# Kernel optimization log

Hardware: AMD Instinct MI355X
Metric: run time of the kernel (lower is better)

The kernel has to match this reference:

```python
import jax, jax.numpy as jnp
import numpy as np

B, T, C = 1, 2048, 2048
H, KV, D = 16, 4, 128
PAST = 2048


def setup_inputs() -> dict:
    key = jax.random.key(0)
    ks = jax.random.split(key, 11)
    return {
        "x": jax.random.normal(ks[0], (B, T, C), jnp.float32),
        "ve": jax.random.normal(ks[1], (B, T, KV * D), jnp.float32),
        "cos": jax.random.normal(ks[2], (1, T, 1, D // 2), jnp.float32),
        "sin": jax.random.normal(ks[3], (1, T, 1, D // 2), jnp.float32),
        "past_key": jax.random.normal(ks[4], (B, PAST, KV, D), jnp.float32),
        "past_value": jax.random.normal(ks[5], (B, PAST, KV, D), jnp.float32),
        "Wq": jax.random.normal(ks[6], (C, H * D), jnp.float32) * 0.02,
        "Wk": jax.random.normal(ks[7], (C, KV * D), jnp.float32) * 0.02,
        "Wv": jax.random.normal(ks[8], (C, KV * D), jnp.float32) * 0.02,
        "Wo": jax.random.normal(ks[9], (H * D, C), jnp.float32) * 0.02,
        "Wg": jax.random.normal(ks[10], (12, KV), jnp.float32),
    }


def _rmsnorm(x):
    return x * jax.lax.rsqrt(jnp.mean(x * x, axis=-1, keepdims=True) + 1e-6)


def _rope(x, cos, sin):
    # x: (B,T,heads,D); cos/sin: (1,T,1,D//2) broadcast over heads
    d = x.shape[-1] // 2
    x1, x2 = x[..., :d], x[..., d:]
    return jnp.concatenate([x1 * cos + x2 * sin, -x1 * sin + x2 * cos], axis=-1)


def reference(x, ve, cos, sin, past_key, past_value, Wq, Wk, Wv, Wo, Wg):
    Bx, Tx, Cx = x.shape
    G = H // KV
    q = (x @ Wq).reshape(Bx, Tx, H, D)
    k = (x @ Wk).reshape(Bx, Tx, KV, D)
    v = (x @ Wv).reshape(Bx, Tx, KV, D)
    # value-embedding gate: 3*sigmoid over first 12 channels of x
    gate = 3.0 * jax.nn.sigmoid(x[..., :12] @ Wg)  # (B,T,KV)
    v = v + gate[..., None] * ve.reshape(Bx, Tx, KV, D)
    q = _rmsnorm(_rope(q, cos, sin)) * 1.2
    k = _rmsnorm(_rope(k, cos, sin)) * 1.2
    present_key = jnp.concatenate([past_key, k], axis=1)    # (B,S,KV,D)
    present_value = jnp.concatenate([past_value, v], axis=1)
    S = present_key.shape[1]
    q_t = q.transpose(0, 2, 1, 3)                           # (B,H,T,D)
    k_t = present_key.transpose(0, 2, 1, 3)                 # (B,KV,S,D)
    v_t = present_value.transpose(0, 2, 1, 3)
    # GQA expansion: repeat each kv head G times -> (B,H,S,D)
    k_t = jnp.broadcast_to(k_t[:, :, None], (Bx, KV, G, S, D)).reshape(Bx, H, S, D)
    v_t = jnp.broadcast_to(v_t[:, :, None], (Bx, KV, G, S, D)).reshape(Bx, H, S, D)
    scale = D ** -0.5
    scores = jnp.einsum("bhtd,bhsd->bhts", q_t, k_t) * scale
    query_pos = jnp.arange(S - Tx, S)[:, None]
    key_pos = jnp.arange(S)[None, :]
    causal = key_pos <= query_pos                           # (T,S)
    scores = jnp.where(causal[None, None], scores, -jnp.inf)
    w = jax.nn.softmax(scores, axis=-1)
    y = jnp.einsum("bhts,bhsd->bthd", w, v_t).reshape(Bx, Tx, H * D)
    y = y @ Wo
    return (y, present_key, present_value)
```

## Files before the change

### kernel.cpp

```cpp
#include <hip/hip_runtime.h>
#include <hip/hip_bf16.h>
#include <math.h>

typedef __attribute__((ext_vector_type(8))) short short8;
typedef __attribute__((ext_vector_type(4))) short short4v;
typedef __attribute__((ext_vector_type(4))) float f32x4;

#define DEV __device__ __forceinline__

DEV short f2bf(float f) {
  unsigned u = __builtin_bit_cast(unsigned, f);
  unsigned r = (u + 0x7FFFu + ((u >> 16) & 1u)) >> 16;
  return (short)r;
}

DEV short f2h(float f) {
  _Float16 h = (_Float16)f;
  return __builtin_bit_cast(short, h);
}

DEV float h2f(short s) {
  return (float)__builtin_bit_cast(_Float16, s);
}

DEV unsigned cvt_pk_bf16(float lo, float hi) {
  unsigned r;
  asm("v_cvt_pk_bf16_f32 %0, %1, %2" : "=v"(r) : "v"(lo), "v"(hi));
  return r;
}

DEV void gload_lds16(const void* g, void* l) {
  __builtin_amdgcn_global_load_lds((const __attribute__((address_space(1))) void*)g,
                                   (__attribute__((address_space(3))) void*)l, 16, 0, 0);
}

__global__ __launch_bounds__(256) void gemm_bf16_m64(const short* __restrict__ A,
                                                     const short* __restrict__ BT,
                                                     float* __restrict__ C,
                                                     int M, int N, int K) {
  __shared__ __attribute__((aligned(16))) short As[2][64 * 64];
  __shared__ __attribute__((aligned(16))) short Bs[2][128 * 64];
  const int tid = threadIdx.x;
  const int w = tid >> 6, l = tid & 63;
  const int g = l >> 4, lr = l & 15;
  int nbx = gridDim.x, nwg = nbx * gridDim.y;
  int flat = blockIdx.y * nbx + blockIdx.x;
  int qq = nwg >> 3;
  int f2 = (flat & 7) * qq + (flat >> 3);
  const int m0 = (f2 / nbx) * 64, n0 = (f2 % nbx) * 128;
  const int wr = w >> 1, wc = w & 1;
  f32x4 acc[2][4] = {};

  auto stage = [&](int buf, int k0) {
#pragma unroll
    for (int it = 0; it < 2; ++it) {
      int idx = it * 256 + tid;
      int row = idx >> 3;
      int scol = ((idx & 7) * 16) ^ ((row & 7) << 4);
      gload_lds16(A + (size_t)(m0 + row) * K + k0 + (scol >> 1), As[buf] + idx * 8);
    }
#pragma unroll
    for (int it = 0; it < 4; ++it) {
      int idx = it * 256 + tid;
      int row = idx >> 3;
      int scol = ((idx & 7) * 16) ^ ((row & 7) << 4);
      gload_lds16(BT + (size_t)(n0 + row) * K + k0 + (scol >> 1), Bs[buf] + idx * 8);
    }
  };

  stage(0, 0);
  __syncthreads();
  int cur = 0;
  for (int k0 = 0; k0 < K; k0 += 64) {
    if (k0 + 64 < K) stage(cur ^ 1, k0 + 64);
#pragma unroll
    for (int ki = 0; ki < 2; ++ki) {
      const int kcol = (ki * 64 + g * 16) ^ ((lr & 7) << 4);
      short8 af[2], bfr[4];
#pragma unroll
      for (int i = 0; i < 2; ++i)
        af[i] = *(const short8*)(As[cur] + (((wr * 32 + i * 16 + lr) * 128 + kcol) >> 1));
#pragma unroll
      for (int i = 0; i < 4; ++i)
        bfr[i] = *(const short8*)(Bs[cur] + (((wc * 64 + i * 16 + lr) * 128 + kcol) >> 1));
#pragma unroll
      for (int mi = 0; mi < 2; ++mi)
#pragma unroll
        for (int ni = 0; ni < 4; ++ni)
          acc[mi][ni] = __builtin_amdgcn_mfma_f32_16x16x32_bf16(af[mi], bfr[ni], acc[mi][ni], 0, 0, 0);
    }
    __syncthreads();
    cur ^= 1;
  }
#pragma unroll
  for (int mi = 0; mi < 2; ++mi)
#pragma unroll
    for (int ni = 0; ni < 4; ++ni) {
      int row = m0 + wr * 32 + mi * 16 + g * 4;
      int col = n0 + wc * 64 + ni * 16 + lr;
#pragma unroll
      for (int r = 0; r < 4; ++r)
        C[(size_t)(row + r) * N + col] = acc[mi][ni][r];
    }
}

__global__ __launch_bounds__(256) void gemm_bf16_k64(const short* __restrict__ A,
                                                     const short* __restrict__ BT,
                                                     float* __restrict__ C,
                                                     int M, int N, int K) {
  __shared__ __attribute__((aligned(16))) short As[2][128 * 64];
  __shared__ __attribute__((aligned(16))) short Bs[2][128 * 64];
  const int tid = threadIdx.x;
  const int w = tid >> 6, l = tid & 63;
  const int g = l >> 4, lr = l & 15;
  int nbx = gridDim.x, nwg = nbx * gridDim.y;
  int flat = blockIdx.y * nbx + blockIdx.x;
  int qq = nwg >> 3;
  int f2 = (flat & 7) * qq + (flat >> 3);
  const int m0 = (f2 / nbx) * 128, n0 = (f2 % nbx) * 128;
  const int wr = w >> 1, wc = w & 1;
  f32x4 acc[4][4] = {};

  auto stage = [&](int buf, int k0) {
#pragma unroll
    for (int it = 0; it < 4; ++it) {
      int idx = it * 256 + tid;
      int row = idx >> 3;
      int colB = (idx & 7) * 16;
      int scol = colB ^ ((row & 7) << 4);
      gload_lds16(A + (size_t)(m0 + row) * K + k0 + (scol >> 1), As[buf] + idx * 8);
      gload_lds16(BT + (size_t)(n0 + row) * K + k0 + (scol >> 1), Bs[buf] + idx * 8);
    }
  };

  stage(0, 0);
  __syncthreads();
  int cur = 0;
  for (int k0 = 0; k0 < K; k0 += 64) {
    if (k0 + 64 < K) stage(cur ^ 1, k0 + 64);
#pragma unroll
    for (int ki = 0; ki < 2; ++ki) {
      short8 af[4], bfr[4];
#pragma unroll
      for (int i = 0; i < 4; ++i) {
        int off = ((wr * 64 + i * 16 + lr) * 128 + ((ki * 64 + g * 16) ^ ((lr & 7) << 4))) >> 1;
        int offb = ((wc * 64 + i * 16 + lr) * 128 + ((ki * 64 + g * 16) ^ ((lr & 7) << 4))) >> 1;
        af[i] = *(const short8*)(As[cur] + off);
        bfr[i] = *(const short8*)(Bs[cur] + offb);
      }
#pragma unroll
      for (int mi = 0; mi < 4; ++mi)
#pragma unroll
        for (int ni = 0; ni < 4; ++ni)
          acc[mi][ni] = __builtin_amdgcn_mfma_f32_16x16x32_bf16(af[mi], bfr[ni], acc[mi][ni], 0, 0, 0);
    }
    __syncthreads();
    cur ^= 1;
  }
#pragma unroll
  for (int mi = 0; mi < 4; ++mi)
#pragma unroll
    for (int ni = 0; ni < 4; ++ni) {
      int row = m0 + wr * 64 + mi * 16 + g * 4;
      int col = n0 + wc * 64 + ni * 16 + lr;
#pragma unroll
      for (int r = 0; r < 4; ++r)
        C[(size_t)(row + r) * N + col] = acc[mi][ni][r];
    }
}

__global__ __launch_bounds__(256) void prep(const float* __restrict__ x,
                                            short* __restrict__ xb,
                                            const float* __restrict__ Wq,
                                            const float* __restrict__ Wk,
                                            const float* __restrict__ Wv,
                                            const float* __restrict__ Wo,
                                            short* __restrict__ WTqkv,
                                            short* __restrict__ WToT) {
  __shared__ float tile[32][33];
  int bid = blockIdx.x;
  int tid = threadIdx.x;
  if (bid < 4096) {
    int i = bid * 256 + tid;
    float4 v = ((const float4*)x)[i];
    short4v o;
    o.x = f2bf(v.x); o.y = f2bf(v.y); o.z = f2bf(v.z); o.w = f2bf(v.w);
    ((short4v*)xb)[i] = o;
    return;
  }
  int b = bid - 4096;
  int bx = b % 160, by = b / 160;
  const float* W;
  short* WT;
  int N, cb;
  if (bx < 64) { W = Wq; WT = WTqkv; N = 2048; cb = bx; }
  else if (bx < 80) { W = Wk; WT = WTqkv + (size_t)2048 * 2048; N = 512; cb = bx - 64; }
  else if (bx < 96) { W = Wv; WT = WTqkv + (size_t)2560 * 2048; N = 512; cb = bx - 80; }
  else { W = Wo; WT = WToT; N = 2048; cb = bx - 96; }
  int tx = tid & 31, ty = tid >> 5;
  int c0 = cb * 32, r0 = by * 32;
#pragma unroll
  for (int i = 0; i < 4; ++i)
    tile[ty + i * 8][tx] = W[(size_t)(r0 + ty + i * 8) * N + c0 + tx];
  __syncthreads();
#pragma unroll
  for (int i = 0; i < 4; ++i)
    WT[(size_t)(c0 + ty + i * 8) * 2048 + r0 + tx] = f2bf(tile[tx][ty + i * 8]);
}

__global__ __launch_bounds__(256) void qkv_post(const float* __restrict__ qkv,
                                                const float* __restrict__ cosb,
                                                const float* __restrict__ sinb,
                                                const float* __restrict__ x,
                                                const float* __restrict__ ve,
                                                const float* __restrict__ Wg,
                                                float* __restrict__ outPK,
                                                float* __restrict__ outPV,
                                                short* __restrict__ qb,
                                                short* __restrict__ kb) {
  int gw = (blockIdx.x * 256 + threadIdx.x) >> 6;
  int l = threadIdx.x & 63;
  int t = gw / 24, u = gw - t * 24;
  if (t >= 2048) return;
  if (u < 20) {
    float c = cosb[t * 64 + l], s = sinb[t * 64 + l];
    const float* src = qkv + (size_t)t * 3072 + (u < 16 ? u * 128 : 2048 + (u - 16) * 128);
    float x1 = src[l], x2 = src[64 + l];
    float lo = x1 * c + x2 * s;
    float hi = x2 * c - x1 * s;
    float ss = lo * lo + hi * hi;
#pragma unroll
    for (int d = 1; d < 64; d <<= 1) ss += __shfl_xor(ss, d, 64);
    float r = rsqrtf(ss * (1.0f / 128.0f) + 1e-6f) * 1.2f;
    if (u < 16) {
      const float SCQ = 0.08838834764831845f * 1.4426950408889634f;
      float rq = r * SCQ;
      size_t b = ((size_t)u * 2048 + t) * 128;
      qb[b + l] = f2bf(lo * rq);
      qb[b + 64 + l] = f2bf(hi * rq);
    } else {
      lo *= r; hi *= r;
      int kvh = u - 16;
      size_t b = ((size_t)(2048 + t) * 4 + kvh) * 128;
      outPK[b + l] = lo;
      outPK[b + 64 + l] = hi;
      size_t b2 = ((size_t)kvh * 4096 + 2048 + t) * 128;
      kb[b2 + l] = f2bf(lo);
      kb[b2 + 64 + l] = f2bf(hi);
    }
  } else {
    int kv = u - 20;
    float z = 0.f;
#pragma unroll
    for (int j = 0; j < 12; ++j) z += x[(size_t)t * 2048 + j] * Wg[j * 4 + kv];
    float gate = 3.0f / (1.0f + expf(-z));
    const float* vr = qkv + (size_t)t * 3072 + 2560 + kv * 128;
    const float* vei = ve + (size_t)t * 512 + kv * 128;
    float v0 = vr[l] + gate * vei[l];
    float v1 = vr[64 + l] + gate * vei[64 + l];
    size_t b = ((size_t)(2048 + t) * 4 + kv) * 128;
    outPV[b + l] = v0;
    outPV[b + 64 + l] = v1;
  }
}

__global__ __launch_bounds__(256) void past_copy(const float* __restrict__ pk,
                                                 const float* __restrict__ pv,
                                                 float* __restrict__ outPK,
                                                 float* __restrict__ outPV,
                                                 short* __restrict__ kb) {
  int i = blockIdx.x * 256 + threadIdx.x;
  int d = i & 127, kv = (i >> 7) & 3, s = i >> 9;
  float a = pk[i], b = pv[i];
  outPK[i] = a;
  outPV[i] = b;
  kb[((size_t)kv * 4096 + s) * 128 + d] = f2bf(a);
}

__global__ __launch_bounds__(256) void v_transpose(const float* __restrict__ PV,
                                                   short* __restrict__ vbT) {
  __shared__ float tile[32][33];
  int tx = threadIdx.x & 31, ty = threadIdx.x >> 5;
  int c0 = blockIdx.x * 32, r0 = blockIdx.y * 32;
#pragma unroll
  for (int i = 0; i < 4; ++i)
    tile[ty + i * 8][tx] = PV[(size_t)(r0 + ty + i * 8) * 512 + c0 + tx];
  __syncthreads();
#pragma unroll
  for (int i = 0; i < 4; ++i)
    vbT[(size_t)(c0 + ty + i * 8) * 4096 + r0 + tx] = f2bf(tile[tx][ty + i * 8]);
}

__global__ __launch_bounds__(256, 2) void attn(const short* __restrict__ qb,
                                               const short* __restrict__ kb,
                                               const short* __restrict__ vbT,
                                               short* __restrict__ Po,
                                               float* __restrict__ ml) {
  extern __shared__ __attribute__((aligned(16))) short smem[];
  short* Ks = smem;
  short* Vs = smem + 16384;
  const int tid = threadIdx.x, w = tid >> 6, l = tid & 63;
  const int g = l >> 4, lr = l & 15;
  const int lid = blockIdx.x;
  const int qbi = 15 - (lid >> 5);
  const int sub = lid & 31;
  const int h = sub >> 1, cls = sub & 1;
  const int kv = h >> 2;
  const int qw = qbi * 128 + w * 32;
  char* Pw = (char*)(smem + 32768) + w * 2048;
  const short* gK = kb + (size_t)kv * 4096 * 128;
  const short* gV = vbT + (size_t)kv * 128 * 4096;
  const int nT = 34 + 2 * qbi;
  const int cnt = (nT - cls + 1) >> 1;

  short8 aq[2][4];
#pragma unroll
  for (int u = 0; u < 2; ++u)
#pragma unroll
    for (int c4 = 0; c4 < 4; ++c4)
      aq[u][c4] = *(const short8*)(qb + ((size_t)(h * 2048 + qw + u * 16 + lr)) * 128 + c4 * 32 + g * 8);

  float m_r[2] = {-INFINITY, -INFINITY};
  float l_r[2] = {0.f, 0.f};
  f32x4 o[2][8] = {};

  const int rK = tid >> 4, cKs = ((tid & 15) * 16) ^ ((rK & 7) << 4);
  const int rV = tid >> 3, cVs = ((tid & 7) * 16) ^ ((rV & 7) << 4);
  const short* kptr = gK + (size_t)(cls * 64 + rK) * 128 + (cKs >> 1);
  const short* vptr = gV + (size_t)rV * 4096 + cls * 64 + (cVs >> 1);
  short* kdst = Ks + w * 512;
  short* vdst = Vs + w * 512;

  auto stageK = [&](int buf) {
#pragma unroll
    for (int it = 0; it < 4; ++it)
      gload_lds16(kptr + it * 2048, kdst + buf * 8192 + it * 2048);
    kptr += 16384;
  };
  auto stageV = [&](int buf) {
#pragma unroll
    for (int it = 0; it < 4; ++it)
      gload_lds16(vptr + (size_t)it * 131072, vdst + buf * 8192 + it * 2048);
    vptr += 128;
  };

  stageK(0);
  stageV(0);
  __syncthreads();
  int cur = 0;
  for (int i = 0; i < cnt; ++i) {
    const int s0 = (cls + 2 * i) * 64;
    if (i + 1 < cnt) {
      stageK(cur ^ 1);
      stageV(cur ^ 1);
    }
    f32x4 sc[2][4] = {};
    __builtin_amdgcn_s_setprio(1);
#pragma unroll
    for (int cc = 0; cc < 4; ++cc) {
      const int rb = cur * 8192 + (cc * 16 + lr) * 128;
      short8 bk[4];
#pragma unroll
      for (int c4 = 0; c4 < 4; ++c4)
        bk[c4] = *(const short8*)(Ks + rb + (((c4 * 64 + g * 16) ^ ((lr & 7) << 4)) >> 1));
#pragma unroll
      for (int c4 = 0; c4 < 4; ++c4) {
        sc[0][cc] = __builtin_amdgcn_mfma_f32_16x16x32_bf16(bk[c4], aq[0][c4], sc[0][cc], 0, 0, 0);
        sc[1][cc] = __builtin_amdgcn_mfma_f32_16x16x32_bf16(bk[c4], aq[1][c4], sc[1][cc], 0, 0, 0);
      }
    }
    __builtin_amdgcn_s_setprio(0);
    if (s0 + 63 > 2048 + qw) {
#pragma unroll
      for (int u = 0; u < 2; ++u)
#pragma unroll
        for (int cc = 0; cc < 4; ++cc)
#pragma unroll
          for (int r = 0; r < 4; ++r)
            sc[u][cc][r] = (s0 + cc * 16 + g * 4 + r <= 2048 + qw + u * 16 + lr)
                               ? sc[u][cc][r] : -INFINITY;
    }
    short8 ap[2][2];
#pragma unroll
    for (int u = 0; u < 2; ++u) {
      float pmax = -INFINITY;
#pragma unroll
      for (int cc = 0; cc < 4; ++cc) {
        float a = fmaxf(fmaxf(sc[u][cc][0], sc[u][cc][1]), fmaxf(sc[u][cc][2], sc[u][cc][3]));
        pmax = fmaxf(pmax, a);
      }
      if (!__all(pmax - m_r[u] <= 8.0f)) {
        float tm = fmaxf(pmax, __shfl_xor(pmax, 16, 64));
        tm = fmaxf(tm, __shfl_xor(tm, 32, 64));
        float mn = fmaxf(m_r[u], tm);
        float corr = exp2f(m_r[u] - mn);
        m_r[u] = mn;
        l_r[u] *= corr;
        float co[4];
#pragma unroll
        for (int r = 0; r < 4; ++r) co[r] = __shfl(corr, (l & 48) | (g * 4 + r), 64);
#pragma unroll
        for (int d8 = 0; d8 < 8; ++d8) {
          f32x4 tt = o[u][d8];
#pragma unroll
          for (int r = 0; r < 4; ++r) tt[r] *= co[r];
          o[u][d8] = tt;
        }
      }
      float ps = 0.f;
#pragma unroll
      for (int cc = 0; cc < 4; ++cc) {
        float p0 = exp2f(sc[u][cc][0] - m_r[u]);
        float p1 = exp2f(sc[u][cc][1] - m_r[u]);
        float p2 = exp2f(sc[u][cc][2] - m_r[u]);
        float p3 = exp2f(sc[u][cc][3] - m_r[u]);
        ps += (p0 + p1) + (p2 + p3);
        unsigned pk0 = cvt_pk_bf16(p0, p1);
        unsigned pk1 = cvt_pk_bf16(p2, p3);
        int off8 = (lr * 128 + cc * 32 + g * 8) ^ ((lr & 7) << 4);
        unsigned long long pq = (unsigned long long)pk0 | ((unsigned long long)pk1 << 32);
        *(unsigned long long*)(Pw + off8) = pq;
      }
      l_r[u] += ps;
#pragma unroll
      for (int ks = 0; ks < 2; ++ks)
        ap[u][ks] = *(const short8*)(Pw + ((lr * 128 + ks * 64 + g * 16) ^ ((lr & 7) << 4)));
    }
    __builtin_amdgcn_s_setprio(1);
#pragma unroll
    for (int d8 = 0; d8 < 8; ++d8) {
      const int rb = cur * 8192 + (d8 * 16 + lr) * 64;
      short8 bv0 = *(const short8*)(Vs + rb + (((0 * 64 + g * 16) ^ ((lr & 7) << 4)) >> 1));
      short8 bv1 = *(const short8*)(Vs + rb + (((1 * 64 + g * 16) ^ ((lr & 7) << 4)) >> 1));
      o[0][d8] = __builtin_amdgcn_mfma_f32_16x16x32_bf16(ap[0][0], bv0, o[0][d8], 0, 0, 0);
      o[0][d8] = __builtin_amdgcn_mfma_f32_16x16x32_bf16(ap[0][1], bv1, o[0][d8], 0, 0, 0);
      o[1][d8] = __builtin_amdgcn_mfma_f32_16x16x32_bf16(ap[1][0], bv0, o[1][d8], 0, 0, 0);
      o[1][d8] = __builtin_amdgcn_mfma_f32_16x16x32_bf16(ap[1][1], bv1, o[1][d8], 0, 0, 0);
    }
    __builtin_amdgcn_s_setprio(0);
    __syncthreads();
    cur ^= 1;
  }
#pragma unroll
  for (int u = 0; u < 2; ++u) {
    float ls = l_r[u];
    ls += __shfl_xor(ls, 16, 64);
    ls += __shfl_xor(ls, 32, 64);
    float inv = 1.0f / ls;
    float invo[4];
#pragma unroll
    for (int r = 0; r < 4; ++r) invo[r] = __shfl(inv, (l & 48) | (g * 4 + r), 64);
#pragma unroll
    for (int d8 = 0; d8 < 8; ++d8)
#pragma unroll
      for (int r = 0; r < 4; ++r)
        Po[((size_t)(cls * 16 + h) * 2048 + qw + u * 16 + g * 4 + r) * 128 + d8 * 16 + lr] =
            f2h(o[u][d8][r] * invo[r]);
    if (g == 0) {
      float2 v;
      v.x = m_r[u];
      v.y = ls;
      ((float2*)ml)[(size_t)(cls * 16 + h) * 2048 + qw + u * 16 + lr] = v;
    }
  }
}

__global__ __launch_bounds__(256) void attn_merge(const short* __restrict__ Po,
                                                  const float* __restrict__ ml,
                                                  short* __restrict__ ya) {
  int i = blockIdx.x * 256 + threadIdx.x;
  int q = i >> 8, rem = i & 255, h = rem >> 4, oct = rem & 15;
  float mc[2], lc[2];
#pragma unroll
  for (int c = 0; c < 2; ++c) {
    float2 v = ((const float2*)ml)[(size_t)(c * 16 + h) * 2048 + q];
    mc[c] = v.x; lc[c] = v.y;
  }
  float m = fmaxf(mc[0], mc[1]);
  float wsum = 0.f, acc[8] = {};
#pragma unroll
  for (int c = 0; c < 2; ++c) {
    float wc = lc[c] * exp2f(mc[c] - m);
    wsum += wc;
    short8 p = *(const short8*)(Po + ((size_t)(c * 16 + h) * 2048 + q) * 128 + oct * 8);
#pragma unroll
    for (int j = 0; j < 8; ++j) acc[j] += wc * h2f(p[j]);
  }
  float inv = 1.0f / wsum;
  short8 ov;
#pragma unroll
  for (int j = 0; j < 8; ++j) ov[j] = f2bf(acc[j] * inv);
  *(short8*)(ya + (size_t)q * 2048 + h * 128 + oct * 8) = ov;
}

extern "C" void kernel_launch(void* const* d_in, const int* in_sizes, int n_in,
                              void* d_out, int out_size, void* d_ws, size_t ws_size,
                              hipStream_t stream) {
  const float* x = (const float*)d_in[0];
  const float* ve = (const float*)d_in[1];
  const float* cosb = (const float*)d_in[2];
  const float* sinb = (const float*)d_in[3];
  const float* past_key = (const float*)d_in[4];
  const float* past_value = (const float*)d_in[5];
  const float* Wq = (const float*)d_in[6];
  const float* Wk = (const float*)d_in[7];
  const float* Wv = (const float*)d_in[8];
  const float* Wo = (const float*)d_in[9];
  const float* Wg = (const float*)d_in[10];

  float* outY = (float*)d_out;
  float* outPK = outY + 4194304;
  float* outPV = outPK + 2097152;

  short* base = (short*)d_ws;
  short* WToT = base;
  short* WTqkv = base + 4194304;
  short* xb = WTqkv + (size_t)6291456;
  float* qkv = (float*)(xb + (size_t)4194304);
  short* qb = (short*)(qkv + (size_t)6291456);
  short* kb = qb + (size_t)4194304;
  short* vbT = kb + (size_t)2097152;
  short* ya = vbT + (size_t)2097152;
  short* Po = WTqkv;
  float* mlb = (float*)(base + 20971520);

  static bool attr_set = false;
  if (!attr_set) {
    (void)hipFuncSetAttribute((const void*)attn,
                              hipFuncAttributeMaxDynamicSharedMemorySize, 73728);
    attr_set = true;
  }

  prep<<<14336, 256, 0, stream>>>(x, xb, Wq, Wk, Wv, Wo, WTqkv, WToT);

  gemm_bf16_m64<<<dim3(24, 32), 256, 0, stream>>>(xb, WTqkv, qkv, 2048, 3072, 2048);

  qkv_post<<<12288, 256, 0, stream>>>(qkv, cosb, sinb, x, ve, Wg, outPK, outPV, qb, kb);
  past_copy<<<4096, 256, 0, stream>>>(past_key, past_value, outPK, outPV, kb);
  v_transpose<<<dim3(16, 128), 256, 0, stream>>>(outPV, vbT);

  attn<<<512, 256, 73728, stream>>>(qb, kb, vbT, Po, mlb);
  attn_merge<<<2048, 256, 0, stream>>>(Po, mlb, ya);

  gemm_bf16_k64<<<dim3(16, 16), 256, 0, stream>>>(ya, WToT, outY, 2048, 2048, 2048);
}
```

Baseline: 181.4 us.

## Emit bf16 QKV from GEMM, fuse past_value copy into transpose, use 64-row output GEMM

The QKV projection GEMM now writes its output in bf16 instead of fp32, which halves the intermediate traffic that qkv_post reads. The past_value copy moves into v_transpose, so the past rows are read once from the input and written to both outputs, rather than copied first and read back. The output projection switches from a 128x128 tile GEMM to a 64x128 tile GEMM, doubling the grid for more parallelism. Rounding the pre-RoPE/RMSNorm q, k, v to bf16 adds precision loss, and v is also written to present_value, so that output loses precision too.

```diff
diff --git a/kernel.cpp b/kernel.cpp
--- a/kernel.cpp
+++ b/kernel.cpp
@@ -14,6 +14,11 @@
   return (short)r;
 }
 
+DEV float bf2f(short s) {
+  unsigned u = ((unsigned)(unsigned short)s) << 16;
+  return __builtin_bit_cast(float, u);
+}
+
 DEV short f2h(float f) {
   _Float16 h = (_Float16)f;
   return __builtin_bit_cast(short, h);
@@ -34,9 +39,79 @@
                                    (__attribute__((address_space(3))) void*)l, 16, 0, 0);
 }
 
-__global__ __launch_bounds__(256) void gemm_bf16_m64(const short* __restrict__ A,
+__global__ __launch_bounds__(256) void gemm_m64_f32(const short* __restrict__ A,
+                                                    const short* __restrict__ BT,
+                                                    float* __restrict__ C,
+                                                    int M, int N, int K) {
+  __shared__ __attribute__((aligned(16))) short As[2][64 * 64];
+  __shared__ __attribute__((aligned(16))) short Bs[2][128 * 64];
+  const int tid = threadIdx.x;
+  const int w = tid >> 6, l = tid & 63;
+  const int g = l >> 4, lr = l & 15;
+  int nbx = gridDim.x, nwg = nbx * gridDim.y;
+  int flat = blockIdx.y * nbx + blockIdx.x;
+  int qq = nwg >> 3;
+  int f2 = (flat & 7) * qq + (flat >> 3);
+  const int m0 = (f2 / nbx) * 64, n0 = (f2 % nbx) * 128;
+  const int wr = w >> 1, wc = w & 1;
+  f32x4 acc[2][4] = {};
+
+  auto stage = [&](int buf, int k0) {
+#pragma unroll
+    for (int it = 0; it < 2; ++it) {
+      int idx = it * 256 + tid;
+      int row = idx >> 3;
+      int scol = ((idx & 7) * 16) ^ ((row & 7) << 4);
+      gload_lds16(A + (size_t)(m0 + row) * K + k0 + (scol >> 1), As[buf] + idx * 8);
+    }
+#pragma unroll
+    for (int it = 0; it < 4; ++it) {
+      int idx = it * 256 + tid;
+      int row = idx >> 3;
+      int scol = ((idx & 7) * 16) ^ ((row & 7) << 4);
+      gload_lds16(BT + (size_t)(n0 + row) * K + k0 + (scol >> 1), Bs[buf] + idx * 8);
+    }
+  };
+
+  stage(0, 0);
+  __syncthreads();
+  int cur = 0;
+  for (int k0 = 0; k0 < K; k0 += 64) {
+    if (k0 + 64 < K) stage(cur ^ 1, k0 + 64);
+#pragma unroll
+    for (int ki = 0; ki < 2; ++ki) {
+      const int kcol = (ki * 64 + g * 16) ^ ((lr & 7) << 4);
+      short8 af[2], bfr[4];
+#pragma unroll
+      for (int i = 0; i < 2; ++i)
+        af[i] = *(const short8*)(As[cur] + (((wr * 32 + i * 16 + lr) * 128 + kcol) >> 1));
+#pragma unroll
+      for (int i = 0; i < 4; ++i)
+        bfr[i] = *(const short8*)(Bs[cur] + (((wc * 64 + i * 16 + lr) * 128 + kcol) >> 1));
+#pragma unroll
+      for (int mi = 0; mi < 2; ++mi)
+#pragma unroll
+        for (int ni = 0; ni < 4; ++ni)
+          acc[mi][ni] = __builtin_amdgcn_mfma_f32_16x16x32_bf16(af[mi], bfr[ni], acc[mi][ni], 0, 0, 0);
+    }
+    __syncthreads();
+    cur ^= 1;
+  }
+#pragma unroll
+  for (int mi = 0; mi < 2; ++mi)
+#pragma unroll
+    for (int ni = 0; ni < 4; ++ni) {
+      int row = m0 + wr * 32 + mi * 16 + g * 4;
+      int col = n0 + wc * 64 + ni * 16 + lr;
+#pragma unroll
+      for (int r = 0; r < 4; ++r)
+        C[(size_t)(row + r) * N + col] = acc[mi][ni][r];
+    }
+}
+
+__global__ __launch_bounds__(256) void gemm_m64_bf16(const short* __restrict__ A,
                                                      const short* __restrict__ BT,
-                                                     float* __restrict__ C,
+                                                     short* __restrict__ C,
                                                      int M, int N, int K) {
   __shared__ __attribute__((aligned(16))) short As[2][64 * 64];
   __shared__ __attribute__((aligned(16))) short Bs[2][128 * 64];
@@ -100,72 +175,7 @@
       int col = n0 + wc * 64 + ni * 16 + lr;
 #pragma unroll
       for (int r = 0; r < 4; ++r)
-        C[(size_t)(row + r) * N + col] = acc[mi][ni][r];
-    }
-}
-
-__global__ __launch_bounds__(256) void gemm_bf16_k64(const short* __restrict__ A,
-                                                     const short* __restrict__ BT,
-                                                     float* __restrict__ C,
-                                                     int M, int N, int K) {
-  __shared__ __attribute__((aligned(16))) short As[2][128 * 64];
-  __shared__ __attribute__((aligned(16))) short Bs[2][128 * 64];
-  const int tid = threadIdx.x;
-  const int w = tid >> 6, l = tid & 63;
-  const int g = l >> 4, lr = l & 15;
-  int nbx = gridDim.x, nwg = nbx * gridDim.y;
-  int flat = blockIdx.y * nbx + blockIdx.x;
-  int qq = nwg >> 3;
-  int f2 = (flat & 7) * qq + (flat >> 3);
-  const int m0 = (f2 / nbx) * 128, n0 = (f2 % nbx) * 128;
-  const int wr = w >> 1, wc = w & 1;
-  f32x4 acc[4][4] = {};
-
-  auto stage = [&](int buf, int k0) {
-#pragma unroll
-    for (int it = 0; it < 4; ++it) {
-      int idx = it * 256 + tid;
-      int row = idx >> 3;
-      int colB = (idx & 7) * 16;
-      int scol = colB ^ ((row & 7) << 4);
-      gload_lds16(A + (size_t)(m0 + row) * K + k0 + (scol >> 1), As[buf] + idx * 8);
-      gload_lds16(BT + (size_t)(n0 + row) * K + k0 + (scol >> 1), Bs[buf] + idx * 8);
-    }
-  };
-
-  stage(0, 0);
-  __syncthreads();
-  int cur = 0;
-  for (int k0 = 0; k0 < K; k0 += 64) {
-    if (k0 + 64 < K) stage(cur ^ 1, k0 + 64);
-#pragma unroll
-    for (int ki = 0; ki < 2; ++ki) {
-      short8 af[4], bfr[4];
-#pragma unroll
-      for (int i = 0; i < 4; ++i) {
-        int off = ((wr * 64 + i * 16 + lr) * 128 + ((ki * 64 + g * 16) ^ ((lr & 7) << 4))) >> 1;
-        int offb = ((wc * 64 + i * 16 + lr) * 128 + ((ki * 64 + g * 16) ^ ((lr & 7) << 4))) >> 1;
-        af[i] = *(const short8*)(As[cur] + off);
-        bfr[i] = *(const short8*)(Bs[cur] + offb);
-      }
-#pragma unroll
-      for (int mi = 0; mi < 4; ++mi)
-#pragma unroll
-        for (int ni = 0; ni < 4; ++ni)
-          acc[mi][ni] = __builtin_amdgcn_mfma_f32_16x16x32_bf16(af[mi], bfr[ni], acc[mi][ni], 0, 0, 0);
-    }
-    __syncthreads();
-    cur ^= 1;
-  }
-#pragma unroll
-  for (int mi = 0; mi < 4; ++mi)
-#pragma unroll
-    for (int ni = 0; ni < 4; ++ni) {
-      int row = m0 + wr * 64 + mi * 16 + g * 4;
-      int col = n0 + wc * 64 + ni * 16 + lr;
-#pragma unroll
-      for (int r = 0; r < 4; ++r)
-        C[(size_t)(row + r) * N + col] = acc[mi][ni][r];
+        C[(size_t)(row + r) * N + col] = f2bf(acc[mi][ni][r]);
     }
 }
 
@@ -208,7 +218,7 @@
     WT[(size_t)(c0 + ty + i * 8) * 2048 + r0 + tx] = f2bf(tile[tx][ty + i * 8]);
 }
 
-__global__ __launch_bounds__(256) void qkv_post(const float* __restrict__ qkv,
+__global__ __launch_bounds__(256) void qkv_post(const short* __restrict__ qkv,
                                                 const float* __restrict__ cosb,
                                                 const float* __restrict__ sinb,
                                                 const float* __restrict__ x,
@@ -224,8 +234,8 @@
   if (t >= 2048) return;
   if (u < 20) {
     float c = cosb[t * 64 + l], s = sinb[t * 64 + l];
-    const float* src = qkv + (size_t)t * 3072 + (u < 16 ? u * 128 : 2048 + (u - 16) * 128);
-    float x1 = src[l], x2 = src[64 + l];
+    const short* src = qkv + (size_t)t * 3072 + (u < 16 ? u * 128 : 2048 + (u - 16) * 128);
+    float x1 = bf2f(src[l]), x2 = bf2f(src[64 + l]);
     float lo = x1 * c + x2 * s;
     float hi = x2 * c - x1 * s;
     float ss = lo * lo + hi * hi;
@@ -254,10 +264,10 @@
 #pragma unroll
     for (int j = 0; j < 12; ++j) z += x[(size_t)t * 2048 + j] * Wg[j * 4 + kv];
     float gate = 3.0f / (1.0f + expf(-z));
-    const float* vr = qkv + (size_t)t * 3072 + 2560 + kv * 128;
+    const short* vr = qkv + (size_t)t * 3072 + 2560 + kv * 128;
     const float* vei = ve + (size_t)t * 512 + kv * 128;
-    float v0 = vr[l] + gate * vei[l];
-    float v1 = vr[64 + l] + gate * vei[64 + l];
+    float v0 = bf2f(vr[l]) + gate * vei[l];
+    float v1 = bf2f(vr[64 + l]) + gate * vei[64 + l];
     size_t b = ((size_t)(2048 + t) * 4 + kv) * 128;
     outPV[b + l] = v0;
     outPV[b + 64 + l] = v1;
@@ -265,26 +275,33 @@
 }
 
 __global__ __launch_bounds__(256) void past_copy(const float* __restrict__ pk,
-                                                 const float* __restrict__ pv,
                                                  float* __restrict__ outPK,
-                                                 float* __restrict__ outPV,
                                                  short* __restrict__ kb) {
   int i = blockIdx.x * 256 + threadIdx.x;
   int d = i & 127, kv = (i >> 7) & 3, s = i >> 9;
-  float a = pk[i], b = pv[i];
+  float a = pk[i];
   outPK[i] = a;
-  outPV[i] = b;
   kb[((size_t)kv * 4096 + s) * 128 + d] = f2bf(a);
 }
 
-__global__ __launch_bounds__(256) void v_transpose(const float* __restrict__ PV,
+__global__ __launch_bounds__(256) void v_transpose(const float* __restrict__ pv,
+                                                   float* __restrict__ outPV,
                                                    short* __restrict__ vbT) {
   __shared__ float tile[32][33];
   int tx = threadIdx.x & 31, ty = threadIdx.x >> 5;
   int c0 = blockIdx.x * 32, r0 = blockIdx.y * 32;
-#pragma unroll
-  for (int i = 0; i < 4; ++i)
-    tile[ty + i * 8][tx] = PV[(size_t)(r0 + ty + i * 8) * 512 + c0 + tx];
+  if (r0 < 2048) {
+#pragma unroll
+    for (int i = 0; i < 4; ++i) {
+      float v = pv[(size_t)(r0 + ty + i * 8) * 512 + c0 + tx];
+      tile[ty + i * 8][tx] = v;
+      outPV[(size_t)(r0 + ty + i * 8) * 512 + c0 + tx] = v;
+    }
+  } else {
+#pragma unroll
+    for (int i = 0; i < 4; ++i)
+      tile[ty + i * 8][tx] = outPV[(size_t)(r0 + ty + i * 8) * 512 + c0 + tx];
+  }
   __syncthreads();
 #pragma unroll
   for (int i = 0; i < 4; ++i)
@@ -516,8 +533,8 @@
   short* WToT = base;
   short* WTqkv = base + 4194304;
   short* xb = WTqkv + (size_t)6291456;
-  float* qkv = (float*)(xb + (size_t)4194304);
-  short* qb = (short*)(qkv + (size_t)6291456);
+  short* qkv = xb + (size_t)4194304;
+  short* qb = qkv + (size_t)12582912;
   short* kb = qb + (size_t)4194304;
   short* vbT = kb + (size_t)2097152;
   short* ya = vbT + (size_t)2097152;
@@ -533,14 +550,14 @@
 
   prep<<<14336, 256, 0, stream>>>(x, xb, Wq, Wk, Wv, Wo, WTqkv, WToT);
 
-  gemm_bf16_m64<<<dim3(24, 32), 256, 0, stream>>>(xb, WTqkv, qkv, 2048, 3072, 2048);
+  gemm_m64_bf16<<<dim3(24, 32), 256, 0, stream>>>(xb, WTqkv, qkv, 2048, 3072, 2048);
 
   qkv_post<<<12288, 256, 0, stream>>>(qkv, cosb, sinb, x, ve, Wg, outPK, outPV, qb, kb);
-  past_copy<<<4096, 256, 0, stream>>>(past_key, past_value, outPK, outPV, kb);
-  v_transpose<<<dim3(16, 128), 256, 0, stream>>>(outPV, vbT);
+  past_copy<<<4096, 256, 0, stream>>>(past_key, outPK, kb);
+  v_transpose<<<dim3(16, 128), 256, 0, stream>>>(past_value, outPV, vbT);
 
   attn<<<512, 256, 73728, stream>>>(qb, kb, vbT, Po, mlb);
   attn_merge<<<2048, 256, 0, stream>>>(Po, mlb, ya);
 
-  gemm_bf16_k64<<<dim3(16, 16), 256, 0, stream>>>(ya, WToT, outY, 2048, 2048, 2048);
-}
+  gemm_m64_f32<<<dim3(16, 32), 256, 0, stream>>>(ya, WToT, outY, 2048, 2048, 2048);
+}
```

Result: no change. 181.0 us (-0.2%).
